# Kernel tuning notes

Hardware: AMD Instinct MI355X
Metric: run time of the kernel (lower is better)

The kernel has to match this reference:

```python
import jax, jax.numpy as jnp
import numpy as np

FILTER = [1.0, 3.0, 3.0, 1.0]
FILTER_RADIUS = len(FILTER) // 2  # = 2


def setup_inputs() -> dict:
    key = jax.random.key(0)
    x = jax.random.normal(key, (16, 128, 128, 128), dtype=jnp.float32)
    # CreateLowpassKernel(Filter, Inplace=True): outer product of the 1-D taps, normalized.
    w = np.array([FILTER], dtype=np.float32)  # [1, 4]
    k = w.T @ w                               # [4, 4]
    kernel = jnp.asarray(k / k.sum(), dtype=jnp.float32)
    return {"x": x, "kernel": kernel}


def pixel_shuffle(x, r):
    # [B, C*r*r, H, W] -> [B, C, H*r, W*r] (torch pixel_shuffle semantics)
    B, C, H, W = x.shape
    c = C // (r * r)
    x = x.reshape(B, c, r, r, H, W)
    x = x.transpose(0, 1, 4, 2, 5, 3)  # B, c, H, r, W, r
    return x.reshape(B, c, H * r, W * r)


def reference(x, kernel):
    # pixel_shuffle by 2, then upfirdn2d(up=1, down=1, padding=FilterRadius):
    # pad by FilterRadius on all sides and apply the 2-D FIR filter as a true
    # convolution (kernel flipped), depthwise across channels.
    x = pixel_shuffle(x, 2)                      # [B, C, 2H, 2W]
    B, C, H, W = x.shape
    f = jnp.flip(kernel, (0, 1))                 # true convolution -> flip taps
    w = jnp.tile(f[None, None], (C, 1, 1, 1))    # [C, 1, kh, kw] depthwise
    p = FILTER_RADIUS
    return jax.lax.conv_general_dilated(
        x, w, window_strides=(1, 1), padding=[(p, p), (p, p)],
        dimension_numbers=("NCHW", "OIHW", "NCHW"),
        feature_group_count=C)  # [B, C, 2H+1, 2W+1]
```

## Files before the change

kernel.cpp:

```cpp
#include <hip/hip_runtime.h>

constexpr int Bn = 16;
constexpr int Hn = 128;
constexpr int Wn = 128;
constexpr int Cc = 32;
constexpr int SH = 2 * Hn;
constexpr int SW = 2 * Wn;
constexpr int OH = SH + 1;
constexpr int OW = SW + 1;
constexpr int HW = Hn * Wn;
constexpr int NG = 33;
constexpr int TY = 9;
constexpr int NSTRIP = (OH + TY - 1) / TY;
constexpr int NTHREADS = Bn * Cc * NG;

__global__ __launch_bounds__(256) void upsamp_fir8(
    const float* __restrict__ x,
    const float* __restrict__ k4,
    float* __restrict__ out)
{
    const int tid = blockIdx.x * 256 + threadIdx.x;
    const int g  = tid % NG;
    const int bc = tid / NG;
    const float* xp = x + (size_t)bc * 4 * HW;

    float fh[4], fv[4];
#pragma unroll
    for (int j = 0; j < 4; ++j) fh[j] = k4[j] + k4[4+j] + k4[8+j] + k4[12+j];
#pragma unroll
    for (int i = 0; i < 4; ++i) fv[i] = k4[4*i] + k4[4*i+1] + k4[4*i+2] + k4[4*i+3];
    const float h0 = fh[3], h1 = fh[2], h2 = fh[1], h3 = fh[0];
    const float g0 = fv[3], g1 = fv[2], g2 = fv[1], g3 = fv[0];

    const int ci  = 4 * g;
    const int aM1 = ci - 1 < 0 ? 0 : ci - 1;
    const int a4  = ci > Wn - 4 ? Wn - 4 : ci;
    const int aP4 = ci + 4 > Wn - 1 ? Wn - 1 : ci + 4;
    float mE[6], mO[5];
#pragma unroll
    for (int i = 0; i < 6; ++i) { int w = 8*g - 2 + 2*i; mE[i] = (unsigned)w < (unsigned)SW ? 1.f : 0.f; }
#pragma unroll
    for (int i = 0; i < 5; ++i) { int w = 8*g - 1 + 2*i; mO[i] = (unsigned)w < (unsigned)SW ? 1.f : 0.f; }

    auto loadrow = [&](int h, float* V) {
        if ((unsigned)h >= (unsigned)SH) {
#pragma unroll
            for (int k = 0; k < 8; ++k) V[k] = 0.f;
            return;
        }
        const float* be = xp + (size_t)(2 * (h & 1)) * HW + (size_t)(h >> 1) * Wn;
        const float* bo = be + HW;
        float E[6], O[5];
        E[0] = be[aM1];
        float4 e4 = *(const float4*)(be + a4);
        E[1] = e4.x; E[2] = e4.y; E[3] = e4.z; E[4] = e4.w;
        E[5] = be[aP4];
        O[0] = bo[aM1];
        float4 o4 = *(const float4*)(bo + a4);
        O[1] = o4.x; O[2] = o4.y; O[3] = o4.z; O[4] = o4.w;
#pragma unroll
        for (int i = 0; i < 6; ++i) E[i] *= mE[i];
#pragma unroll
        for (int i = 0; i < 5; ++i) O[i] *= mO[i];
#pragma unroll
        for (int k = 0; k < 8; k += 2) {
            int i = k >> 1;
            V[k]   = h0*E[i] + h1*O[i]   + h2*E[i+1] + h3*O[i+1];
            V[k+1] = h0*O[i] + h1*E[i+1] + h2*O[i+1] + h3*E[i+2];
        }
    };

    const int oh0 = blockIdx.y * TY;
    float va[8], vb[8], vc[8], vd[8];
    loadrow(oh0 - 2, va);
    loadrow(oh0 - 1, vb);
    loadrow(oh0,     vc);

    float* op = out + ((size_t)bc * OH + oh0) * OW + 8 * g;
    const int tmax = (OH - oh0) < TY ? (OH - oh0) : TY;
#pragma unroll 3
    for (int t = 0; t < tmax; ++t) {
        loadrow(oh0 + t + 1, vd);
        float o[8];
#pragma unroll
        for (int k = 0; k < 8; ++k)
            o[k] = g0*va[k] + g1*vb[k] + g2*vc[k] + g3*vd[k];
        float* p = op + (size_t)t * OW;
        if (g < NG - 1) {
#pragma unroll
            for (int k = 0; k < 8; ++k) p[k] = o[k];
        } else {
            p[0] = o[0];
        }
#pragma unroll
        for (int k = 0; k < 8; ++k) { va[k] = vb[k]; vb[k] = vc[k]; vc[k] = vd[k]; }
    }
}

extern "C" void kernel_launch(void* const* d_in, const int* in_sizes, int n_in,
                              void* d_out, int out_size, void* d_ws, size_t ws_size,
                              hipStream_t stream)
{
    const float* x  = (const float*)d_in[0];
    const float* k4 = (const float*)d_in[1];
    float* out      = (float*)d_out;

    dim3 grid(NTHREADS / 256, NSTRIP, 1);
    upsamp_fir8<<<grid, dim3(256), 0, stream>>>(x, k4, out);
}
```

Baseline: 277.6 us.

## Stage input rows through LDS with one output column per thread and register prefetch

Replaces the per-thread 8-column register scheme with a block-per-(batch,channel) layout. Each block's 256 threads stage one even and one odd input row into double-buffered LDS, then each thread computes one output column. Rows are prefetched four steps ahead in registers, and tall 65-row strips keep the vertical filter in a sliding register window. The aim is coalesced scalar loads and stores and less redundant global reads, at the cost of a __syncthreads per output row and a single edge thread handling column 256.

```diff
diff --git a/kernel.cpp b/kernel.cpp
--- a/kernel.cpp
+++ b/kernel.cpp
@@ -1,27 +1,25 @@
 #include <hip/hip_runtime.h>
 
-constexpr int Bn = 16;
 constexpr int Hn = 128;
 constexpr int Wn = 128;
-constexpr int Cc = 32;
 constexpr int SH = 2 * Hn;
-constexpr int SW = 2 * Wn;
 constexpr int OH = SH + 1;
-constexpr int OW = SW + 1;
+constexpr int OW = 257;
 constexpr int HW = Hn * Wn;
-constexpr int NG = 33;
-constexpr int TY = 9;
-constexpr int NSTRIP = (OH + TY - 1) / TY;
-constexpr int NTHREADS = Bn * Cc * NG;
+constexpr int TY = 65;
+constexpr int NSTRIP = 4;
+constexpr int NBC = 16 * 32;
+constexpr int PF = 4;
+constexpr int NIT = TY + 3;
 
-__global__ __launch_bounds__(256) void upsamp_fir8(
+__global__ __launch_bounds__(256, 8) void upsamp_fir_lds(
     const float* __restrict__ x,
     const float* __restrict__ k4,
     float* __restrict__ out)
 {
-    const int tid = blockIdx.x * 256 + threadIdx.x;
-    const int g  = tid % NG;
-    const int bc = tid / NG;
+    const int tix = threadIdx.x;
+    const int bc  = blockIdx.x;
+    const int oh0 = blockIdx.y * TY;
     const float* xp = x + (size_t)bc * 4 * HW;
 
     float fh[4], fv[4];
@@ -32,68 +30,72 @@
     const float h0 = fh[3], h1 = fh[2], h2 = fh[1], h3 = fh[0];
     const float g0 = fv[3], g1 = fv[2], g2 = fv[1], g3 = fv[0];
 
-    const int ci  = 4 * g;
-    const int aM1 = ci - 1 < 0 ? 0 : ci - 1;
-    const int a4  = ci > Wn - 4 ? Wn - 4 : ci;
-    const int aP4 = ci + 4 > Wn - 1 ? Wn - 1 : ci + 4;
-    float mE[6], mO[5];
-#pragma unroll
-    for (int i = 0; i < 6; ++i) { int w = 8*g - 2 + 2*i; mE[i] = (unsigned)w < (unsigned)SW ? 1.f : 0.f; }
-#pragma unroll
-    for (int i = 0; i < 5; ++i) { int w = 8*g - 1 + 2*i; mO[i] = (unsigned)w < (unsigned)SW ? 1.f : 0.f; }
+    __shared__ float lds[2][2][132];
+    if (tix < 8) {
+        int b = tix >> 2, r = tix & 3;
+        lds[b][r >> 1][(r & 1) ? 129 : 0] = 0.f;
+    }
 
-    auto loadrow = [&](int h, float* V) {
-        if ((unsigned)h >= (unsigned)SH) {
-#pragma unroll
-            for (int k = 0; k < 8; ++k) V[k] = 0.f;
-            return;
-        }
-        const float* be = xp + (size_t)(2 * (h & 1)) * HW + (size_t)(h >> 1) * Wn;
-        const float* bo = be + HW;
-        float E[6], O[5];
-        E[0] = be[aM1];
-        float4 e4 = *(const float4*)(be + a4);
-        E[1] = e4.x; E[2] = e4.y; E[3] = e4.z; E[4] = e4.w;
-        E[5] = be[aP4];
-        O[0] = bo[aM1];
-        float4 o4 = *(const float4*)(bo + a4);
-        O[1] = o4.x; O[2] = o4.y; O[3] = o4.z; O[4] = o4.w;
-#pragma unroll
-        for (int i = 0; i < 6; ++i) E[i] *= mE[i];
-#pragma unroll
-        for (int i = 0; i < 5; ++i) O[i] *= mO[i];
-#pragma unroll
-        for (int k = 0; k < 8; k += 2) {
-            int i = k >> 1;
-            V[k]   = h0*E[i] + h1*O[i]   + h2*E[i+1] + h3*O[i+1];
-            V[k+1] = h0*O[i] + h1*E[i+1] + h2*O[i+1] + h3*E[i+2];
-        }
+    const int eo       = tix < 128 ? 0 : 1;
+    const int lane     = tix & 127;
+    const int stageIdx = 1 + lane;
+
+    auto xload = [&](int s) -> float {
+        return xp[(size_t)(2 * (s & 1) + eo) * HW + (size_t)(s >> 1) * Wn + lane];
     };
 
-    const int oh0 = blockIdx.y * TY;
-    float va[8], vb[8], vc[8], vd[8];
-    loadrow(oh0 - 2, va);
-    loadrow(oh0 - 1, vb);
-    loadrow(oh0,     vc);
+    const int c    = tix;
+    const int mi   = c >> 1;
+    const int codd = c & 1;
+    const bool edge = (tix == 255);
 
-    float* op = out + ((size_t)bc * OH + oh0) * OW + 8 * g;
-    const int tmax = (OH - oh0) < TY ? (OH - oh0) : TY;
-#pragma unroll 3
-    for (int t = 0; t < tmax; ++t) {
-        loadrow(oh0 + t + 1, vd);
-        float o[8];
-#pragma unroll
-        for (int k = 0; k < 8; ++k)
-            o[k] = g0*va[k] + g1*vb[k] + g2*vc[k] + g3*vd[k];
-        float* p = op + (size_t)t * OW;
-        if (g < NG - 1) {
-#pragma unroll
-            for (int k = 0; k < 8; ++k) p[k] = o[k];
-        } else {
-            p[0] = o[0];
+    float* const obase = out + (size_t)bc * OH * OW;
+
+    float rr0 = 0, rr1 = 0, rr2 = 0, rr3 = 0;
+    { int s = oh0 - 2; if ((unsigned)s < (unsigned)SH) rr0 = xload(s); }
+    { int s = oh0 - 1; if ((unsigned)s < (unsigned)SH) rr1 = xload(s); }
+    { int s = oh0;     if ((unsigned)s < (unsigned)SH) rr2 = xload(s); }
+    { int s = oh0 + 1; if ((unsigned)s < (unsigned)SH) rr3 = xload(s); }
+
+    float hm3 = 0, hm2 = 0, hm1 = 0;
+    float em3 = 0, em2 = 0, em1 = 0;
+
+    auto step = [&](int m, float& rr, int buf) {
+        const int s = oh0 - 2 + m;
+        lds[buf][eo][stageIdx] = rr;
+        float nv = 0.f;
+        const int sp = s + PF;
+        if (m < NIT - PF && sp < SH) nv = xload(sp);
+        rr = nv;
+        __syncthreads();
+        const float* EB = lds[buf][0];
+        const float* OB = lds[buf][1];
+        const float* P = codd ? (OB + mi) : (EB + mi);
+        const float* Q = codd ? (EB + mi + 1) : (OB + mi);
+        const float p0 = P[0], p1 = P[1];
+        const float q0 = Q[0], q1 = Q[1];
+        const float hn = h0*p0 + h1*q0 + h2*p1 + h3*q1;
+        float en = 0.f;
+        if (edge) {
+            en = h0*EB[128] + h1*OB[128] + h2*EB[129] + h3*OB[129];
         }
-#pragma unroll
-        for (int k = 0; k < 8; ++k) { va[k] = vb[k]; vb[k] = vc[k]; vc[k] = vd[k]; }
+        if (m >= 3) {
+            const int oh = oh0 + m - 3;
+            if (oh < OH) {
+                float* p = obase + (size_t)oh * OW;
+                p[c] = g0*hm3 + g1*hm2 + g2*hm1 + g3*hn;
+                if (edge) p[256] = g0*em3 + g1*em2 + g2*em1 + g3*en;
+            }
+        }
+        hm3 = hm2; hm2 = hm1; hm1 = hn;
+        em3 = em2; em2 = em1; em1 = en;
+    };
+
+    for (int mm = 0; mm < NIT; mm += 4) {
+        step(mm + 0, rr0, 0);
+        step(mm + 1, rr1, 1);
+        step(mm + 2, rr2, 0);
+        step(mm + 3, rr3, 1);
     }
 }
 
@@ -105,6 +107,6 @@
     const float* k4 = (const float*)d_in[1];
     float* out      = (float*)d_out;
 
-    dim3 grid(NTHREADS / 256, NSTRIP, 1);
-    upsamp_fir8<<<grid, dim3(256), 0, stream>>>(x, k4, out);
+    dim3 grid(NBC, NSTRIP, 1);
+    upsamp_fir_lds<<<grid, dim3(256), 0, stream>>>(x, k4, out);
 }
```

Measured after the change: 249.0 us. 10.3% less time.
